# Optimization experiments

Hardware: AMD Instinct MI355X
Metric: run time of the kernel (lower is better)

## Reference

```python
import jax, jax.numpy as jnp
import numpy as np

# Physical constants hardcoded in the torch module: m=[1.0, 50.0], l=[1.0, 1.0], g=10.0
M_DIAG = jnp.array([1.0, 1.0, 50.0, 50.0], dtype=jnp.float32)  # mass matrix diagonal [m0,m0,m1,m1]
G = 10.0


def _phi(x):
    # x: [4] = (x0, y0, x1, y1); two holonomic rod-length constraints
    c1 = x[0] ** 2 + x[1] ** 2 - 1.0
    c2 = (x[0] - x[2]) ** 2 + (x[1] - x[3]) ** 2 - 1.0
    return jnp.stack([c1, c2])  # [2]


def _potential(x):
    # U = sum_i m_i * g * y_i  (y coords are x[1], x[3])
    return M_DIAG[0] * G * x[1] + M_DIAG[2] * G * x[3]


def _forward(coords):
    x, v = jnp.split(coords, 2, axis=-1)  # each [bs, 4]
    minv = (1.0 / M_DIAG).astype(coords.dtype)  # diagonal of M^{-1}, [4]

    # phi_q[:, i] = d phi_i / dx  -> [bs, 2, 4]
    phi_q = jax.vmap(jax.jacfwd(_phi))(x)

    # phi_qq[:, i] = d/dx ( phi_q[i] . v )  -> [bs, 2, 4]
    def _gdot(xi, vi):
        return jax.jacfwd(_phi)(xi) @ vi  # [2]

    phi_qq = jax.vmap(jax.jacfwd(_gdot, argnums=0))(x, v)

    # F = -dV/dx  -> [bs, 4]
    F = -jax.vmap(jax.grad(_potential))(x)

    # Minv is diagonal: phi_q @ Minv == phi_q * minv (broadcast over last axis)
    phiq_Minv = phi_q * minv  # [bs, 2, 4]

    L = jnp.einsum('bik,bjk->bij', phiq_Minv, phi_q)  # [bs, 2, 2]
    R = jnp.einsum('bik,bk->bi', phiq_Minv, F) + jnp.einsum('bik,bk->bi', phi_qq, v)  # [bs, 2]
    lam = jnp.einsum('bij,bj->bi', jnp.linalg.inv(L), R)  # [bs, 2]

    a = minv * (F - jnp.einsum('bik,bi->bk', phi_q, lam))  # [bs, 4]
    return jnp.concatenate([v, a], axis=-1)  # [bs, 8]


def setup_inputs() -> dict:
    key = jax.random.key(0)
    coords = jax.random.normal(key, (2097152, 8), dtype=jnp.float32)
    t = jnp.zeros((1,), dtype=jnp.float32)
    return {"t": t, "coords": coords}


def reference(t, coords):
    # t is unused in the dynamics (autonomous system), matching the torch forward
    return _forward(coords)
```

## Files before the change

### kernel.cpp

```cpp
#include <hip/hip_runtime.h>


__global__ __launch_bounds__(256) void pend2_dae_kernel(
    const float4* __restrict__ in,
    float4* __restrict__ out,
    int n)
{
    int i = blockIdx.x * blockDim.x + threadIdx.x;
    if (i >= n) return;

    float4 p = in[2 * i];
    float4 q = in[2 * i + 1];

    float x0 = p.x, y0 = p.y, x1 = p.z, y1 = p.w;
    float u0 = q.x, w0 = q.y, u1 = q.z, w1 = q.w;

    float dx = x0 - x1, dy = y0 - y1;
    float du = u0 - u1, dw = w0 - w1;

    float L11 = 4.0f * (x0 * x0 + y0 * y0);
    float L12 = 4.0f * (x0 * dx + y0 * dy);
    float L22 = 4.08f * (dx * dx + dy * dy);

    float R1 = -20.0f * y0 + 2.0f * (u0 * u0 + w0 * w0);
    float R2 = 2.0f * (du * du + dw * dw);

    float det = L11 * L22 - L12 * L12;
    float inv = 1.0f / det;
    float lam1 = (L22 * R1 - L12 * R2) * inv;
    float lam2 = (L11 * R2 - L12 * R1) * inv;

    float a0 = -2.0f * (x0 * lam1 + dx * lam2);
    float a1 = -10.0f - 2.0f * (y0 * lam1 + dy * lam2);
    float a2 = 0.04f * dx * lam2;
    float a3 = -10.0f + 0.04f * dy * lam2;

    out[2 * i]     = q;
    out[2 * i + 1] = make_float4(a0, a1, a2, a3);
}

extern "C" void kernel_launch(void* const* d_in, const int* in_sizes, int n_in,
                              void* d_out, int out_size, void* d_ws, size_t ws_size,
                              hipStream_t stream) {
    const float4* coords = (const float4*)d_in[1];
    float4* out = (float4*)d_out;
    int n = in_sizes[1] / 8;

    int block = 256;
    int grid = (n + block - 1) / block;
    pend2_dae_kernel<<<grid, block, 0, stream>>>(coords, out, n);
}
```

Measured before the change: 115.6 us.

## Use one float4 per thread with lane shuffles and nontemporal stores

Each thread now loads a single contiguous float4 and swaps it with its neighbour lane through xor shuffles, so a pair of threads rebuilds one sample. Loads and stores become fully contiguous per wavefront instead of strided by two float4s. The output is written with nontemporal stores to reduce cache pollution. The cost is twice as many threads, duplicated arithmetic in both lanes of each pair, and extra shuffle instructions.

```diff
diff --git a/kernel.cpp b/kernel.cpp
--- a/kernel.cpp
+++ b/kernel.cpp
@@ -1,16 +1,27 @@
 #include <hip/hip_runtime.h>
 
+
+typedef float vfloat4_t __attribute__((ext_vector_type(4)));
 
 __global__ __launch_bounds__(256) void pend2_dae_kernel(
     const float4* __restrict__ in,
     float4* __restrict__ out,
-    int n)
+    int n4)
 {
-    int i = blockIdx.x * blockDim.x + threadIdx.x;
-    if (i >= n) return;
+    int j = blockIdx.x * blockDim.x + threadIdx.x;
+    if (j >= n4) return;
 
-    float4 p = in[2 * i];
-    float4 q = in[2 * i + 1];
+    float4 mine = in[j];
+
+    float4 other;
+    other.x = __shfl_xor(mine.x, 1);
+    other.y = __shfl_xor(mine.y, 1);
+    other.z = __shfl_xor(mine.z, 1);
+    other.w = __shfl_xor(mine.w, 1);
+
+    bool odd = (j & 1);
+    float4 p = odd ? other : mine;
+    float4 q = odd ? mine : other;
 
     float x0 = p.x, y0 = p.y, x1 = p.z, y1 = p.w;
     float u0 = q.x, w0 = q.y, u1 = q.z, w1 = q.w;
@@ -30,13 +41,17 @@
     float lam1 = (L22 * R1 - L12 * R2) * inv;
     float lam2 = (L11 * R2 - L12 * R1) * inv;
 
-    float a0 = -2.0f * (x0 * lam1 + dx * lam2);
-    float a1 = -10.0f - 2.0f * (y0 * lam1 + dy * lam2);
-    float a2 = 0.04f * dx * lam2;
-    float a3 = -10.0f + 0.04f * dy * lam2;
+    vfloat4_t res;
+    if (odd) {
+        res.x = -2.0f * (x0 * lam1 + dx * lam2);
+        res.y = -10.0f - 2.0f * (y0 * lam1 + dy * lam2);
+        res.z = 0.04f * dx * lam2;
+        res.w = -10.0f + 0.04f * dy * lam2;
+    } else {
+        res.x = q.x; res.y = q.y; res.z = q.z; res.w = q.w;
+    }
 
-    out[2 * i]     = q;
-    out[2 * i + 1] = make_float4(a0, a1, a2, a3);
+    __builtin_nontemporal_store(res, (vfloat4_t*)&out[j]);
 }
 
 extern "C" void kernel_launch(void* const* d_in, const int* in_sizes, int n_in,
@@ -44,9 +59,9 @@
                               hipStream_t stream) {
     const float4* coords = (const float4*)d_in[1];
     float4* out = (float4*)d_out;
-    int n = in_sizes[1] / 8;
+    int n4 = in_sizes[1] / 4;
 
     int block = 256;
-    int grid = (n + block - 1) / block;
-    pend2_dae_kernel<<<grid, block, 0, stream>>>(coords, out, n);
+    int grid = (n4 + block - 1) / block;
+    pend2_dae_kernel<<<grid, block, 0, stream>>>(coords, out, n4);
 }
```

After: 109.7 us. 1.05x faster.
